# Kernel tuning notes

Hardware: AMD Instinct MI355X
Metric: run time of the kernel (lower is better)

Reference implementation:

```python
import jax, jax.numpy as jnp
import numpy as np

N_ATOMS = 10000
N_EDGES = 320000
F = 128
LN_EPS = 1e-5
VN_EPS = 1e-8


def _layer_norm(x, gamma, beta):
    mu = jnp.mean(x, axis=-1, keepdims=True)
    var = jnp.mean(jnp.square(x - mu), axis=-1, keepdims=True)
    return (x - mu) * jax.lax.rsqrt(var + LN_EPS) * gamma + beta


def _vector_norm(x):
    # Equivariant RMS normalization: per-channel vector norms, RMS over channels.
    sq = jnp.sum(jnp.square(x), axis=1, keepdims=True)          # [N,1,F]
    rms = jnp.sqrt(jnp.mean(sq, axis=-1, keepdims=True) + VN_EPS)  # [N,1,1]
    return x / rms


def setup_inputs() -> dict:
    key = jax.random.key(0)
    ks = jax.random.split(key, 16)
    rn = lambda k, shape, s=1.0: jax.random.normal(k, shape, dtype=jnp.float32) * s
    w_s = 0.05  # small init scale for weights
    return {
        "h": rn(ks[0], (N_ATOMS, 1, F)),
        "v": rn(ks[1], (N_ATOMS, 3, F)),
        "H": rn(ks[2], (N_ATOMS, 1, F)),
        "V": rn(ks[3], (N_ATOMS, 3, F)),
        "Wij": rn(ks[4], (N_EDGES, 1, 3 * F)),
        "dir_ij": rn(ks[5], (N_EDGES, 3)),
        "W1": rn(ks[6], (F, F), w_s),
        "b1": jnp.zeros((F,), jnp.float32),
        "W2": rn(ks[7], (F, 3 * F), w_s),
        "b2": jnp.zeros((3 * F,), jnp.float32),
        "Wmix": rn(ks[8], (F, 2 * F), w_s),
        "Wh_remain": rn(ks[9], (F, F), w_s),
        "Wh_forget": rn(ks[10], (F, F), w_s),
        "Wv_remain": rn(ks[11], (F, 1), w_s),
        "gamma": jnp.ones((F,), jnp.float32),
        "beta": jnp.zeros((F,), jnp.float32),
        "idx_i": jnp.sort(jax.random.randint(ks[12], (N_EDGES,), 0, N_ATOMS)),
        "idx_j": jax.random.randint(ks[13], (N_EDGES,), 0, N_ATOMS),
        "n_atoms": N_ATOMS,
    }


def reference(h, v, H, V, Wij, dir_ij, W1, b1, W2, b2, Wmix,
              Wh_remain, Wh_forget, Wv_remain, gamma, beta,
              idx_i, idx_j, n_atoms):
    # interatomic context net: Dense(F,F,silu) -> Dense(F,3F)
    X = jax.nn.silu(H @ W1 + b1) @ W2 + b2            # [N,1,3F]
    Hj = X[idx_j]                                      # [E,1,3F]
    Vj = V[idx_j]                                      # [E,3,F]
    Xe = Wij * Hj                                      # [E,1,3F]
    dh_e, dvR, dvv = jnp.split(Xe, 3, axis=-1)         # each [E,1,F]
    dh = jax.ops.segment_sum(dh_e, idx_i, num_segments=n_atoms)  # [N,1,F]
    dv_e = dvR * dir_ij[:, :, None] + dvv * Vj         # [E,3,F]
    dv = jax.ops.segment_sum(dv_e, idx_i, num_segments=n_atoms)  # [N,3,F]

    v_mix = v @ Wmix                                   # [N,3,2F]
    v_V, v_W = jnp.split(v_mix, 2, axis=-1)
    ctx = jnp.sum(v_V * v_W, axis=1, keepdims=True)    # [N,1,F]

    q = _layer_norm(h + dh @ Wh_remain + (dh @ Wh_forget) * ctx, gamma, beta)
    mu = _vector_norm(v + dv + (dh @ Wv_remain) * v)
    return q, mu
```

## Files before the change

kernel.cpp:

```cpp
#include <hip/hip_runtime.h>
#include <math.h>

#define FDIM 128
#define F3   384

static constexpr int K1_R = 8;
static constexpr int K2_R = 8;
static constexpr int K4_R = 4;
static constexpr int CHUNK = 64;

__global__ __launch_bounds__(256) void k0_seg(
    const int* __restrict__ idx_i, int* __restrict__ seg, int E, int N)
{
    int n = blockIdx.x * 256 + threadIdx.x;
    if (n > N) return;
    if (n == N) { seg[n] = E; return; }
    int lo = 0, hi = E;
    while (lo < hi) {
        int m = (lo + hi) >> 1;
        if (idx_i[m] < n) lo = m + 1; else hi = m;
    }
    seg[n] = lo;
}

__global__ __launch_bounds__(128) void k1_ctxnet(
    const float* __restrict__ H,  const float* __restrict__ W1,
    const float* __restrict__ b1, const float* __restrict__ W2,
    const float* __restrict__ b2, float* __restrict__ X, int N)
{
    __shared__ float sH[K1_R][FDIM];
    __shared__ float sT[K1_R][FDIM];
    const int f  = threadIdx.x;
    const int n0 = blockIdx.x * K1_R;

    for (int r = 0; r < K1_R; ++r) {
        int n = n0 + r;
        sH[r][f] = (n < N) ? H[(size_t)n * FDIM + f] : 0.f;
    }
    __syncthreads();

    float acc[K1_R];
    #pragma unroll
    for (int r = 0; r < K1_R; ++r) acc[r] = 0.f;
    #pragma unroll 4
    for (int a = 0; a < FDIM; ++a) {
        float w = W1[a * FDIM + f];
        #pragma unroll
        for (int r = 0; r < K1_R; ++r) acc[r] = fmaf(sH[r][a], w, acc[r]);
    }
    float bb = b1[f];
    #pragma unroll
    for (int r = 0; r < K1_R; ++r) {
        float t = acc[r] + bb;
        sT[r][f] = t / (1.f + expf(-t));
    }
    __syncthreads();

    float a0[K1_R], a1[K1_R], a2[K1_R];
    #pragma unroll
    for (int r = 0; r < K1_R; ++r) { a0[r] = 0.f; a1[r] = 0.f; a2[r] = 0.f; }
    #pragma unroll 4
    for (int a = 0; a < FDIM; ++a) {
        float w0 = W2[a * F3 + f];
        float w1 = W2[a * F3 + FDIM + f];
        float w2 = W2[a * F3 + 2 * FDIM + f];
        #pragma unroll
        for (int r = 0; r < K1_R; ++r) {
            float t = sT[r][a];
            a0[r] = fmaf(t, w0, a0[r]);
            a1[r] = fmaf(t, w1, a1[r]);
            a2[r] = fmaf(t, w2, a2[r]);
        }
    }
    float c0 = b2[f], c1 = b2[FDIM + f], c2 = b2[2 * FDIM + f];
    for (int r = 0; r < K1_R; ++r) {
        int n = n0 + r;
        if (n < N) {
            X[(size_t)n * F3 + f]            = a0[r] + c0;
            X[(size_t)n * F3 + FDIM + f]     = a1[r] + c1;
            X[(size_t)n * F3 + 2 * FDIM + f] = a2[r] + c2;
        }
    }
}

__global__ __launch_bounds__(128) void k2_ctx(
    const float* __restrict__ v, const float* __restrict__ Wmix,
    float* __restrict__ ctx, int N)
{
    __shared__ float sv[3][K2_R][FDIM];
    const int f  = threadIdx.x;
    const int n0 = blockIdx.x * K2_R;

    for (int r = 0; r < K2_R; ++r) {
        int n = n0 + r;
        for (int d = 0; d < 3; ++d)
            sv[d][r][f] = (n < N) ? v[((size_t)n * 3 + d) * FDIM + f] : 0.f;
    }
    __syncthreads();

    float cacc[K2_R];
    #pragma unroll
    for (int r = 0; r < K2_R; ++r) cacc[r] = 0.f;

    for (int d = 0; d < 3; ++d) {
        float aV[K2_R], aW[K2_R];
        #pragma unroll
        for (int r = 0; r < K2_R; ++r) { aV[r] = 0.f; aW[r] = 0.f; }
        #pragma unroll 4
        for (int a = 0; a < FDIM; ++a) {
            float w0 = Wmix[a * (2 * FDIM) + f];
            float w1 = Wmix[a * (2 * FDIM) + FDIM + f];
            #pragma unroll
            for (int r = 0; r < K2_R; ++r) {
                float t = sv[d][r][a];
                aV[r] = fmaf(t, w0, aV[r]);
                aW[r] = fmaf(t, w1, aW[r]);
            }
        }
        #pragma unroll
        for (int r = 0; r < K2_R; ++r) cacc[r] = fmaf(aV[r], aW[r], cacc[r]);
    }
    for (int r = 0; r < K2_R; ++r) {
        int n = n0 + r;
        if (n < N) ctx[(size_t)n * FDIM + f] = cacc[r];
    }
}

__global__ __launch_bounds__(256) void k3_edges(
    const float* __restrict__ X, const float* __restrict__ V,
    const float* __restrict__ Wij, const float* __restrict__ dir_ij,
    const int* __restrict__ seg, const int* __restrict__ idx_j,
    float* __restrict__ dh, float* __restrict__ dv)
{
    const int n    = blockIdx.x;
    const int tid  = threadIdx.x;
    const int f    = tid & 127;
    const int half = tid >> 7;

    __shared__ int   sj[CHUNK];
    __shared__ float sd[CHUNK][4];
    __shared__ float sacc[4][FDIM];

    const int e0 = seg[n];
    const int e1 = seg[n + 1];

    float adh = 0.f, a0 = 0.f, a1 = 0.f, a2 = 0.f;

#define EDGE_LOAD(kk, W0,W1_,W2_,X0,X1,X2,V0,V1,V2,D0,D1,D2)                   \
    {   const int e_ = base + (kk); const int j_ = sj[(kk)];                   \
        const float* w_ = Wij + (size_t)e_ * F3;                               \
        const float* x_ = X   + (size_t)j_ * F3;                               \
        const float* q_ = V   + (size_t)j_ * F3;                               \
        W0 = __builtin_nontemporal_load(w_ + f);                               \
        W1_ = __builtin_nontemporal_load(w_ + FDIM + f);                       \
        W2_ = __builtin_nontemporal_load(w_ + 2 * FDIM + f);                   \
        X0 = x_[f]; X1 = x_[FDIM + f]; X2 = x_[2 * FDIM + f];                  \
        V0 = q_[f]; V1 = q_[FDIM + f]; V2 = q_[2 * FDIM + f];                  \
        D0 = sd[(kk)][0]; D1 = sd[(kk)][1]; D2 = sd[(kk)][2]; }

#define EDGE_FMA(W0,W1_,W2_,X0,X1,X2,V0,V1,V2,D0,D1,D2)                       \
    {   adh = fmaf(W0, X0, adh);                                               \
        float r_ = W1_ * X1, s_ = W2_ * X2;                                    \
        a0 = fmaf(r_, D0, fmaf(s_, V0, a0));                                   \
        a1 = fmaf(r_, D1, fmaf(s_, V1, a1));                                   \
        a2 = fmaf(r_, D2, fmaf(s_, V2, a2)); }

    for (int base = e0; base < e1; base += CHUNK) {
        const int cnt = (e1 - base < CHUNK) ? (e1 - base) : CHUNK;
        if (tid < cnt) sj[tid] = idx_j[base + tid];
        for (int t = tid; t < 3 * cnt; t += 256)
            sd[t / 3][t % 3] = dir_ij[(size_t)base * 3 + t];
        __syncthreads();

        int k = half;
        for (; k + 6 < cnt; k += 8) {
            float wA0,wA1,wA2,xA0,xA1,xA2,vA0,vA1,vA2,dA0,dA1,dA2;
            float wB0,wB1,wB2,xB0,xB1,xB2,vB0,vB1,vB2,dB0,dB1,dB2;
            float wC0,wC1,wC2,xC0,xC1,xC2,vC0,vC1,vC2,dC0,dC1,dC2;
            float wD0,wD1,wD2,xD0,xD1,xD2,vD0,vD1,vD2,dD0,dD1,dD2;
            EDGE_LOAD(k,     wA0,wA1,wA2,xA0,xA1,xA2,vA0,vA1,vA2,dA0,dA1,dA2)
            EDGE_LOAD(k + 2, wB0,wB1,wB2,xB0,xB1,xB2,vB0,vB1,vB2,dB0,dB1,dB2)
            EDGE_LOAD(k + 4, wC0,wC1,wC2,xC0,xC1,xC2,vC0,vC1,vC2,dC0,dC1,dC2)
            EDGE_LOAD(k + 6, wD0,wD1,wD2,xD0,xD1,xD2,vD0,vD1,vD2,dD0,dD1,dD2)
            EDGE_FMA(wA0,wA1,wA2,xA0,xA1,xA2,vA0,vA1,vA2,dA0,dA1,dA2)
            EDGE_FMA(wB0,wB1,wB2,xB0,xB1,xB2,vB0,vB1,vB2,dB0,dB1,dB2)
            EDGE_FMA(wC0,wC1,wC2,xC0,xC1,xC2,vC0,vC1,vC2,dC0,dC1,dC2)
            EDGE_FMA(wD0,wD1,wD2,xD0,xD1,xD2,vD0,vD1,vD2,dD0,dD1,dD2)
        }
        for (; k < cnt; k += 2) {
            float w0,w1,w2,x0,x1,x2,v0,v1,v2,d0,d1,d2;
            EDGE_LOAD(k, w0,w1,w2,x0,x1,x2,v0,v1,v2,d0,d1,d2)
            EDGE_FMA(w0,w1,w2,x0,x1,x2,v0,v1,v2,d0,d1,d2)
        }
        __syncthreads();
    }
#undef EDGE_LOAD
#undef EDGE_FMA

    if (half == 1) {
        sacc[0][f] = adh; sacc[1][f] = a0; sacc[2][f] = a1; sacc[3][f] = a2;
    }
    __syncthreads();
    if (half == 0) {
        adh += sacc[0][f]; a0 += sacc[1][f]; a1 += sacc[2][f]; a2 += sacc[3][f];
        dh[(size_t)n * FDIM + f]          = adh;
        dv[(size_t)n * F3 + f]            = a0;
        dv[(size_t)n * F3 + FDIM + f]     = a1;
        dv[(size_t)n * F3 + 2 * FDIM + f] = a2;
    }
}

__device__ inline float block_reduce_sum_128(float val, float* tmp) {
    #pragma unroll
    for (int o = 32; o > 0; o >>= 1) val += __shfl_down(val, o, 64);
    const int tid = threadIdx.x;
    if ((tid & 63) == 0) tmp[tid >> 6] = val;
    __syncthreads();
    float r = tmp[0] + tmp[1];
    __syncthreads();
    return r;
}

__global__ __launch_bounds__(128) void k4_epilogue(
    const float* __restrict__ h,   const float* __restrict__ v,
    const float* __restrict__ dh,  const float* __restrict__ dv,
    const float* __restrict__ ctx,
    const float* __restrict__ Whr, const float* __restrict__ Whf,
    const float* __restrict__ Wvr,
    const float* __restrict__ gamma, const float* __restrict__ beta,
    float* __restrict__ q, float* __restrict__ mu, int N)
{
    __shared__ float sdh[K4_R][FDIM];
    __shared__ float sred[2];
    const int f  = threadIdx.x;
    const int n0 = blockIdx.x * K4_R;

    for (int r = 0; r < K4_R; ++r) {
        int n = n0 + r;
        sdh[r][f] = (n < N) ? dh[(size_t)n * FDIM + f] : 0.f;
    }
    __syncthreads();

    float accR[K4_R], accF[K4_R];
    #pragma unroll
    for (int r = 0; r < K4_R; ++r) { accR[r] = 0.f; accF[r] = 0.f; }
    #pragma unroll 4
    for (int a = 0; a < FDIM; ++a) {
        float wr = Whr[a * FDIM + f];
        float wf = Whf[a * FDIM + f];
        #pragma unroll
        for (int r = 0; r < K4_R; ++r) {
            accR[r] = fmaf(sdh[r][a], wr, accR[r]);
            accF[r] = fmaf(sdh[r][a], wf, accF[r]);
        }
    }

    const float wv = Wvr[f];
    const float g  = gamma[f];
    const float bt = beta[f];

    for (int r = 0; r < K4_R; ++r) {
        int n = n0 + r;
        if (n >= N) break;

        float s = block_reduce_sum_128(sdh[r][f] * wv, sred);

        float u    = h[(size_t)n * FDIM + f] + accR[r] + accF[r] * ctx[(size_t)n * FDIM + f];
        float mean = block_reduce_sum_128(u, sred) * (1.f / 128.f);
        float dlt  = u - mean;
        float var  = block_reduce_sum_128(dlt * dlt, sred) * (1.f / 128.f);
        q[(size_t)n * FDIM + f] = dlt * rsqrtf(var + 1e-5f) * g + bt;

        float sc = 1.f + s;
        float x0 = fmaf(v[((size_t)n * 3 + 0) * FDIM + f], sc, dv[(size_t)n * F3 + f]);
        float x1 = fmaf(v[((size_t)n * 3 + 1) * FDIM + f], sc, dv[(size_t)n * F3 + FDIM + f]);
        float x2 = fmaf(v[((size_t)n * 3 + 2) * FDIM + f], sc, dv[(size_t)n * F3 + 2 * FDIM + f]);
        float sq  = x0 * x0 + x1 * x1 + x2 * x2;
        float tot = block_reduce_sum_128(sq, sred) * (1.f / 128.f);
        float inv = rsqrtf(tot + 1e-8f);
        mu[((size_t)n * 3 + 0) * FDIM + f] = x0 * inv;
        mu[((size_t)n * 3 + 1) * FDIM + f] = x1 * inv;
        mu[((size_t)n * 3 + 2) * FDIM + f] = x2 * inv;
    }
}

extern "C" void kernel_launch(void* const* d_in, const int* in_sizes, int n_in,
                              void* d_out, int out_size, void* d_ws, size_t ws_size,
                              hipStream_t stream)
{
    const float* h     = (const float*)d_in[0];
    const float* v     = (const float*)d_in[1];
    const float* H     = (const float*)d_in[2];
    const float* V     = (const float*)d_in[3];
    const float* Wij   = (const float*)d_in[4];
    const float* dir   = (const float*)d_in[5];
    const float* W1    = (const float*)d_in[6];
    const float* b1    = (const float*)d_in[7];
    const float* W2    = (const float*)d_in[8];
    const float* b2    = (const float*)d_in[9];
    const float* Wmix  = (const float*)d_in[10];
    const float* Whr   = (const float*)d_in[11];
    const float* Whf   = (const float*)d_in[12];
    const float* Wvr   = (const float*)d_in[13];
    const float* gamma = (const float*)d_in[14];
    const float* beta  = (const float*)d_in[15];
    const int*   idx_i = (const int*)d_in[16];
    const int*   idx_j = (const int*)d_in[17];

    const int N = in_sizes[0] / FDIM;
    const int E = in_sizes[16];

    float* ws  = (float*)d_ws;
    float* X   = ws;
    float* ctx = X   + (size_t)N * F3;
    float* dh  = ctx + (size_t)N * FDIM;
    float* dv  = dh  + (size_t)N * FDIM;
    int*   seg = (int*)(dv + (size_t)N * F3);

    float* q   = (float*)d_out;
    float* mu  = q + (size_t)N * FDIM;

    hipLaunchKernelGGL(k0_seg, dim3((N + 256) / 256), dim3(256), 0, stream,
                       idx_i, seg, E, N);
    hipLaunchKernelGGL(k1_ctxnet, dim3((N + K1_R - 1) / K1_R), dim3(128), 0, stream,
                       H, W1, b1, W2, b2, X, N);
    hipLaunchKernelGGL(k2_ctx, dim3((N + K2_R - 1) / K2_R), dim3(128), 0, stream,
                       v, Wmix, ctx, N);
    hipLaunchKernelGGL(k3_edges, dim3(N), dim3(256), 0, stream,
                       X, V, Wij, dir, seg, idx_j, dh, dv);
    hipLaunchKernelGGL(k4_epilogue, dim3((N + K4_R - 1) / K4_R), dim3(128), 0, stream,
                       h, v, dh, dv, ctx, Whr, Whf, Wvr, gamma, beta, q, mu, N);
}
```

Before: 885.5 us.

## Vectorize edge kernel to float4 loads with 8 edge groups per block

Result: no change. 888.3 us (+0.3%).

```diff
diff --git a/kernel.cpp b/kernel.cpp
--- a/kernel.cpp
+++ b/kernel.cpp
@@ -8,6 +8,25 @@
 static constexpr int K2_R = 8;
 static constexpr int K4_R = 4;
 static constexpr int CHUNK = 64;
+
+typedef float vf4 __attribute__((ext_vector_type(4)));
+
+__device__ __forceinline__ vf4 fma4(vf4 a, vf4 b, vf4 c) {
+    vf4 r;
+    r[0] = fmaf(a[0], b[0], c[0]);
+    r[1] = fmaf(a[1], b[1], c[1]);
+    r[2] = fmaf(a[2], b[2], c[2]);
+    r[3] = fmaf(a[3], b[3], c[3]);
+    return r;
+}
+__device__ __forceinline__ vf4 fma4s(vf4 a, float s, vf4 c) {
+    vf4 r;
+    r[0] = fmaf(a[0], s, c[0]);
+    r[1] = fmaf(a[1], s, c[1]);
+    r[2] = fmaf(a[2], s, c[2]);
+    r[3] = fmaf(a[3], s, c[3]);
+    return r;
+}
 
 __global__ __launch_bounds__(256) void k0_seg(
     const int* __restrict__ idx_i, int* __restrict__ seg, int E, int N)
@@ -132,38 +151,22 @@
     const int* __restrict__ seg, const int* __restrict__ idx_j,
     float* __restrict__ dh, float* __restrict__ dv)
 {
-    const int n    = blockIdx.x;
-    const int tid  = threadIdx.x;
-    const int f    = tid & 127;
-    const int half = tid >> 7;
+    const int n   = blockIdx.x;
+    const int tid = threadIdx.x;
+    const int g   = tid >> 5;
+    const int l   = tid & 31;
 
     __shared__ int   sj[CHUNK];
     __shared__ float sd[CHUNK][4];
-    __shared__ float sacc[4][FDIM];
+    __shared__ vf4   sacc[8][4][32];
 
     const int e0 = seg[n];
     const int e1 = seg[n + 1];
 
-    float adh = 0.f, a0 = 0.f, a1 = 0.f, a2 = 0.f;
-
-#define EDGE_LOAD(kk, W0,W1_,W2_,X0,X1,X2,V0,V1,V2,D0,D1,D2)                   \
-    {   const int e_ = base + (kk); const int j_ = sj[(kk)];                   \
-        const float* w_ = Wij + (size_t)e_ * F3;                               \
-        const float* x_ = X   + (size_t)j_ * F3;                               \
-        const float* q_ = V   + (size_t)j_ * F3;                               \
-        W0 = __builtin_nontemporal_load(w_ + f);                               \
-        W1_ = __builtin_nontemporal_load(w_ + FDIM + f);                       \
-        W2_ = __builtin_nontemporal_load(w_ + 2 * FDIM + f);                   \
-        X0 = x_[f]; X1 = x_[FDIM + f]; X2 = x_[2 * FDIM + f];                  \
-        V0 = q_[f]; V1 = q_[FDIM + f]; V2 = q_[2 * FDIM + f];                  \
-        D0 = sd[(kk)][0]; D1 = sd[(kk)][1]; D2 = sd[(kk)][2]; }
-
-#define EDGE_FMA(W0,W1_,W2_,X0,X1,X2,V0,V1,V2,D0,D1,D2)                       \
-    {   adh = fmaf(W0, X0, adh);                                               \
-        float r_ = W1_ * X1, s_ = W2_ * X2;                                    \
-        a0 = fmaf(r_, D0, fmaf(s_, V0, a0));                                   \
-        a1 = fmaf(r_, D1, fmaf(s_, V1, a1));                                   \
-        a2 = fmaf(r_, D2, fmaf(s_, V2, a2)); }
+    vf4 adh = {0.f, 0.f, 0.f, 0.f};
+    vf4 a0  = {0.f, 0.f, 0.f, 0.f};
+    vf4 a1  = {0.f, 0.f, 0.f, 0.f};
+    vf4 a2  = {0.f, 0.f, 0.f, 0.f};
 
     for (int base = e0; base < e1; base += CHUNK) {
         const int cnt = (e1 - base < CHUNK) ? (e1 - base) : CHUNK;
@@ -172,41 +175,83 @@
             sd[t / 3][t % 3] = dir_ij[(size_t)base * 3 + t];
         __syncthreads();
 
-        int k = half;
-        for (; k + 6 < cnt; k += 8) {
-            float wA0,wA1,wA2,xA0,xA1,xA2,vA0,vA1,vA2,dA0,dA1,dA2;
-            float wB0,wB1,wB2,xB0,xB1,xB2,vB0,vB1,vB2,dB0,dB1,dB2;
-            float wC0,wC1,wC2,xC0,xC1,xC2,vC0,vC1,vC2,dC0,dC1,dC2;
-            float wD0,wD1,wD2,xD0,xD1,xD2,vD0,vD1,vD2,dD0,dD1,dD2;
-            EDGE_LOAD(k,     wA0,wA1,wA2,xA0,xA1,xA2,vA0,vA1,vA2,dA0,dA1,dA2)
-            EDGE_LOAD(k + 2, wB0,wB1,wB2,xB0,xB1,xB2,vB0,vB1,vB2,dB0,dB1,dB2)
-            EDGE_LOAD(k + 4, wC0,wC1,wC2,xC0,xC1,xC2,vC0,vC1,vC2,dC0,dC1,dC2)
-            EDGE_LOAD(k + 6, wD0,wD1,wD2,xD0,xD1,xD2,vD0,vD1,vD2,dD0,dD1,dD2)
-            EDGE_FMA(wA0,wA1,wA2,xA0,xA1,xA2,vA0,vA1,vA2,dA0,dA1,dA2)
-            EDGE_FMA(wB0,wB1,wB2,xB0,xB1,xB2,vB0,vB1,vB2,dB0,dB1,dB2)
-            EDGE_FMA(wC0,wC1,wC2,xC0,xC1,xC2,vC0,vC1,vC2,dC0,dC1,dC2)
-            EDGE_FMA(wD0,wD1,wD2,xD0,xD1,xD2,vD0,vD1,vD2,dD0,dD1,dD2)
-        }
-        for (; k < cnt; k += 2) {
-            float w0,w1,w2,x0,x1,x2,v0,v1,v2,d0,d1,d2;
-            EDGE_LOAD(k, w0,w1,w2,x0,x1,x2,v0,v1,v2,d0,d1,d2)
-            EDGE_FMA(w0,w1,w2,x0,x1,x2,v0,v1,v2,d0,d1,d2)
+        int kk = g;
+        for (; kk + 8 < cnt; kk += 16) {
+            const int eA = base + kk,     jA = sj[kk];
+            const int eB = base + kk + 8, jB = sj[kk + 8];
+            const vf4* wA = (const vf4*)(Wij + (size_t)eA * F3);
+            const vf4* xA = (const vf4*)(X   + (size_t)jA * F3);
+            const vf4* qA = (const vf4*)(V   + (size_t)jA * F3);
+            const vf4* wB = (const vf4*)(Wij + (size_t)eB * F3);
+            const vf4* xB = (const vf4*)(X   + (size_t)jB * F3);
+            const vf4* qB = (const vf4*)(V   + (size_t)jB * F3);
+
+            vf4 wA0 = __builtin_nontemporal_load(wA + l);
+            vf4 wA1 = __builtin_nontemporal_load(wA + 32 + l);
+            vf4 wA2 = __builtin_nontemporal_load(wA + 64 + l);
+            vf4 xA0 = xA[l], xA1 = xA[32 + l], xA2 = xA[64 + l];
+            vf4 vA0 = qA[l], vA1 = qA[32 + l], vA2 = qA[64 + l];
+            vf4 wB0 = __builtin_nontemporal_load(wB + l);
+            vf4 wB1 = __builtin_nontemporal_load(wB + 32 + l);
+            vf4 wB2 = __builtin_nontemporal_load(wB + 64 + l);
+            vf4 xB0 = xB[l], xB1 = xB[32 + l], xB2 = xB[64 + l];
+            vf4 vB0 = qB[l], vB1 = qB[32 + l], vB2 = qB[64 + l];
+
+            const float dA0 = sd[kk][0],     dA1 = sd[kk][1],     dA2 = sd[kk][2];
+            const float dB0 = sd[kk + 8][0], dB1 = sd[kk + 8][1], dB2 = sd[kk + 8][2];
+
+            adh = fma4(wA0, xA0, adh);
+            {
+                vf4 r = wA1 * xA1, s = wA2 * xA2;
+                a0 = fma4s(r, dA0, fma4(s, vA0, a0));
+                a1 = fma4s(r, dA1, fma4(s, vA1, a1));
+                a2 = fma4s(r, dA2, fma4(s, vA2, a2));
+            }
+            adh = fma4(wB0, xB0, adh);
+            {
+                vf4 r = wB1 * xB1, s = wB2 * xB2;
+                a0 = fma4s(r, dB0, fma4(s, vB0, a0));
+                a1 = fma4s(r, dB1, fma4(s, vB1, a1));
+                a2 = fma4s(r, dB2, fma4(s, vB2, a2));
+            }
+        }
+        for (; kk < cnt; kk += 8) {
+            const int e = base + kk, j = sj[kk];
+            const vf4* w = (const vf4*)(Wij + (size_t)e * F3);
+            const vf4* x = (const vf4*)(X   + (size_t)j * F3);
+            const vf4* q = (const vf4*)(V   + (size_t)j * F3);
+            vf4 w0 = __builtin_nontemporal_load(w + l);
+            vf4 w1 = __builtin_nontemporal_load(w + 32 + l);
+            vf4 w2 = __builtin_nontemporal_load(w + 64 + l);
+            vf4 x0 = x[l], x1 = x[32 + l], x2 = x[64 + l];
+            vf4 v0 = q[l], v1 = q[32 + l], v2 = q[64 + l];
+            const float d0 = sd[kk][0], d1 = sd[kk][1], d2 = sd[kk][2];
+
+            adh = fma4(w0, x0, adh);
+            vf4 r = w1 * x1, s = w2 * x2;
+            a0 = fma4s(r, d0, fma4(s, v0, a0));
+            a1 = fma4s(r, d1, fma4(s, v1, a1));
+            a2 = fma4s(r, d2, fma4(s, v2, a2));
         }
         __syncthreads();
     }
-#undef EDGE_LOAD
-#undef EDGE_FMA
-
-    if (half == 1) {
-        sacc[0][f] = adh; sacc[1][f] = a0; sacc[2][f] = a1; sacc[3][f] = a2;
-    }
-    __syncthreads();
-    if (half == 0) {
-        adh += sacc[0][f]; a0 += sacc[1][f]; a1 += sacc[2][f]; a2 += sacc[3][f];
-        dh[(size_t)n * FDIM + f]          = adh;
-        dv[(size_t)n * F3 + f]            = a0;
-        dv[(size_t)n * F3 + FDIM + f]     = a1;
-        dv[(size_t)n * F3 + 2 * FDIM + f] = a2;
+
+    sacc[g][0][l] = adh;
+    sacc[g][1][l] = a0;
+    sacc[g][2][l] = a1;
+    sacc[g][3][l] = a2;
+    __syncthreads();
+
+    if (tid < 128) {
+        const int c  = tid >> 5;
+        const int ll = tid & 31;
+        vf4 s = sacc[0][c][ll];
+        #pragma unroll
+        for (int gg = 1; gg < 8; ++gg) s += sacc[gg][c][ll];
+        if (c == 0)
+            ((vf4*)(dh + (size_t)n * FDIM))[ll] = s;
+        else
+            ((vf4*)(dv + (size_t)n * F3))[(c - 1) * 32 + ll] = s;
     }
 }
 
```
